# Kernel tuning notes

Hardware: AMD Instinct MI355X
Metric: run time of the kernel (lower is better)

The kernel has to match this reference:

```python
import jax, jax.numpy as jnp
import numpy as np

BS, V, S, K = 4, 2048, 7, 10
CLASS_NUM, VEC_NUM, CAT = 6, 8, 16
OUT_HEAD = CLASS_NUM + VEC_NUM * 3  # 30
DIM_FUSE = 128 + 128 + 256 + 256 + 512 + 512 + 16  # 1808


def _normalize(x, axis):
    return x / jnp.maximum(jnp.linalg.norm(x, axis=axis, keepdims=True), 1e-12)


def knn_index(verts, k):
    # verts: (b, v, 3) -> (b, v, k) excluding self
    inner = jnp.einsum('bnd,bmd->bnm', verts, verts)
    sq = jnp.sum(verts * verts, axis=2)
    dist = sq[:, :, None] + sq[:, None, :] - 2.0 * inner
    _, idx = jax.lax.top_k(-dist, k + 1)
    return idx[:, :, 1:]


def nearest_index(target, source):
    # target: (b, v1, 3), source: (b, v2, 3) -> (b, v1)
    inner = jnp.einsum('bnd,bmd->bnm', target, source)
    d = jnp.sum(source * source, 2)[:, None, :] + jnp.sum(target * target, 2)[:, :, None] - 2.0 * inner
    return jnp.argmin(d, axis=-1)


def gather_nb(t, idx):
    # t: (b, v, d), idx: (b, v1, k) -> (b, v1, k, d)
    return jax.vmap(lambda tt, ii: tt[ii])(t, idx)


def gather1(t, idx):
    # t: (b, v, d), idx: (b, v1) -> (b, v1, d)
    return jax.vmap(lambda tt, ii: tt[ii])(t, idx)


def bn_train(x, g, b, eps=1e-5):
    # x: (b, v, c); BatchNorm1d training-mode over (batch, vertices)
    m = jnp.mean(x, axis=(0, 1), keepdims=True)
    v = jnp.var(x, axis=(0, 1), keepdims=True)
    return (x - m) * jax.lax.rsqrt(v + eps) * g + b


def conv_surface(nb_idx, verts, directions, s, kernel_num):
    nd = _normalize(gather_nb(verts, nb_idx) - verts[:, :, None, :], -1)  # (b,v,n,3)
    sd = _normalize(directions, 0)  # (3, s*k)
    theta = jax.nn.relu(jnp.einsum('bvnd,dk->bvnk', nd, sd))
    b_, v_, n_, _ = theta.shape
    theta = theta.reshape(b_, v_, n_, s, kernel_num)
    return jnp.sum(jnp.max(theta, axis=2), axis=2)  # (b, v, kernel_num)


def conv_layer(nb_idx, verts, fm, w, b, directions, s, out_ch):
    nd = _normalize(gather_nb(verts, nb_idx) - verts[:, :, None, :], -1)
    sd = _normalize(directions, 0)  # (3, s*out_ch)
    theta = jax.nn.relu(jnp.einsum('bvnd,dk->bvnk', nd, sd))  # (b,v,n,s*o)
    fo = jnp.einsum('bvc,ck->bvk', fm, w) + b  # (b, v, (s+1)*o)
    center = fo[..., :out_ch]
    supp = gather_nb(fo[..., out_ch:], nb_idx)  # (b,v,n,s*o)
    act = (theta * supp).reshape(theta.shape[0], theta.shape[1], theta.shape[2], s, out_ch)
    act = jnp.sum(jnp.max(act, axis=2), axis=2)  # (b, v, o)
    return center + act


def pool_layer(verts, fm, pooling_rate, nb_num):
    idx = knn_index(verts, nb_num)
    pooled = jnp.max(gather_nb(fm, idx), axis=2)
    pool_num = verts.shape[1] // pooling_rate
    # deterministic subsample (torch uses randperm; fixed arange for reproducibility)
    return verts[:, :pool_num], pooled[:, :pool_num]


def setup_inputs() -> dict:
    key = jax.random.key(0)
    ks = jax.random.split(key, 16)
    def rn(i, shape, scale=0.05):
        return jax.random.normal(ks[i], shape, dtype=jnp.float32) * scale
    z = lambda *s: jnp.zeros(s, jnp.float32)
    o = lambda *s: jnp.ones(s, jnp.float32)
    return {
        'vertices': jax.random.normal(ks[0], (BS, V, 3), dtype=jnp.float32),
        'onehot': jax.nn.one_hot(jax.random.randint(ks[1], (BS,), 0, CAT), CAT, dtype=jnp.float32),
        'dir0': rn(2, (3, S * 128)),
        'w1': rn(3, (128, (S + 1) * 128)), 'b1': z((S + 1) * 128), 'dir1': rn(4, (3, S * 128)),
        'w2': rn(5, (128, (S + 1) * 256)), 'b2': z((S + 1) * 256), 'dir2': rn(6, (3, S * 256)),
        'w3': rn(7, (256, (S + 1) * 256)), 'b3': z((S + 1) * 256), 'dir3': rn(8, (3, S * 256)),
        'w4': rn(9, (256, (S + 1) * 512)), 'b4': z((S + 1) * 512), 'dir4': rn(10, (3, S * 512)),
        'g_bn1': o(128), 'be_bn1': z(128),
        'g_bn2': o(256), 'be_bn2': z(256),
        'g_bn3': o(256), 'be_bn3': z(256),
        'wc1': rn(11, (512, DIM_FUSE)), 'bc1': z(512),
        'wc2': rn(12, (512, 512)), 'bc2': z(512),
        'wc3': rn(13, (OUT_HEAD, 512)), 'bc3': z(OUT_HEAD),
    }


def reference(vertices, onehot, dir0, w1, b1, dir1, w2, b2, dir2, w3, b3, dir3,
              w4, b4, dir4, g_bn1, be_bn1, g_bn2, be_bn2, g_bn3, be_bn3,
              wc1, bc1, wc2, bc2, wc3, bc3):
    bs, v_num, _ = vertices.shape
    nb = knn_index(vertices, K)
    fm0 = jax.nn.relu(conv_surface(nb, vertices, dir0, S, 128))
    fm1 = jax.nn.relu(bn_train(conv_layer(nb, vertices, fm0, w1, b1, dir1, S, 128), g_bn1, be_bn1))
    vp1, fp1 = pool_layer(vertices, fm1, 4, 4)
    nb1 = knn_index(vp1, min(K, vp1.shape[1] // 8))
    fm2 = jax.nn.relu(bn_train(conv_layer(nb1, vp1, fp1, w2, b2, dir2, S, 256), g_bn2, be_bn2))
    fm3 = jax.nn.relu(bn_train(conv_layer(nb1, vp1, fm2, w3, b3, dir3, S, 256), g_bn3, be_bn3))
    vp2, fp2 = pool_layer(vp1, fm3, 4, 4)
    nb2 = knn_index(vp2, min(K, vp2.shape[1] // 8))
    fm4 = conv_layer(nb2, vp2, fp2, w4, b4, dir4, S, 512)
    f_global = jnp.max(fm4, axis=1)  # (b, 512)
    n1 = nearest_index(vertices, vp1)
    n2 = nearest_index(vertices, vp2)
    fm2u = gather1(fm2, n1)
    fm3u = gather1(fm3, n1)
    fm4u = gather1(fm4, n2)
    fg = jnp.broadcast_to(f_global[:, None, :], (bs, v_num, 512))
    oh = jnp.broadcast_to(onehot[:, None, :], (bs, v_num, CAT))
    feat = jnp.concatenate([fm0, fm1, fm2u, fm3u, fm4u, oh], axis=2)
    fuse = jnp.concatenate([fm0, fm1, fm2u, fm3u, fm4u, fg, oh], axis=2)
    h = jax.nn.relu(jnp.einsum('bvc,oc->bvo', fuse, wc1) + bc1)
    h = jax.nn.relu(jnp.einsum('bvc,oc->bvo', h, wc2) + bc2)
    pred = jnp.einsum('bvc,oc->bvo', h, wc3) + bc3
    seg = pred[..., :CLASS_NUM]
    vecs = pred[..., CLASS_NUM:CLASS_NUM + VEC_NUM * 3]
    return (seg, vecs, feat)
```

## Files before the change

### kernel.cpp

```cpp
#include <hip/hip_runtime.h>
#include <hip/hip_bf16.h>
#include <math.h>

#define BSZ 4
#define VN 2048
#define SS 7
#define KNB 10

typedef __attribute__((ext_vector_type(8))) short short8;
typedef __attribute__((ext_vector_type(4))) float f32x4;
typedef __attribute__((address_space(1))) const void gcvoid;
typedef __attribute__((address_space(3))) void lvoid;

__device__ inline ushort f2bf(float x) {
    __hip_bfloat16 h = __float2bfloat16(x);
    return *(ushort*)&h;
}

__device__ inline void gl2lds16(const ushort* g, ushort* l) {
    __builtin_amdgcn_global_load_lds((gcvoid*)g, (lvoid*)l, 16, 0, 0);
}

__device__ inline unsigned fenc(float f) {
    unsigned b = __float_as_uint(f);
    return (b & 0x80000000u) ? ~b : (b | 0x80000000u);
}
__device__ inline float fdec(unsigned e) {
    unsigned b = (e & 0x80000000u) ? (e & 0x7FFFFFFFu) : ~e;
    return __uint_as_float(b);
}

#define INS(dq, iq, dd, jj) { bool lt_ = (dd) < (dq); \
    float dmn_ = lt_ ? (dd) : (dq); float dmx_ = lt_ ? (dq) : (dd); \
    int imn_ = lt_ ? (jj) : (iq); int imx_ = lt_ ? (iq) : (jj); \
    (dq) = dmn_; (iq) = imn_; (dd) = dmx_; (jj) = imx_; }

#define PB0 8960L
#define PB1 24320L
#define PB2 958208L
#define PB3 1220352L

__global__ void prep_uber(const float* __restrict__ d0, const float* __restrict__ d1,
                          const float* __restrict__ d2, const float* __restrict__ d3,
                          const float* __restrict__ d4,
                          float* __restrict__ s0, float* __restrict__ s1,
                          float* __restrict__ s2, float* __restrict__ s3, float* __restrict__ s4,
                          const float* __restrict__ wc3, float* __restrict__ wc3t,
                          const float* __restrict__ wc1, ushort* __restrict__ wc1b,
                          const float* __restrict__ wc2, ushort* __restrict__ wc2b) {
    long i = blockIdx.x * 256L + threadIdx.x;
    if (i < PB0) {
        const float* src; float* dst; int C, c;
        if (i < 896)        { src = d0; dst = s0; C = 896;  c = (int)i; }
        else if (i < 1792)  { src = d1; dst = s1; C = 896;  c = (int)i - 896; }
        else if (i < 3584)  { src = d2; dst = s2; C = 1792; c = (int)i - 1792; }
        else if (i < 5376)  { src = d3; dst = s3; C = 1792; c = (int)i - 3584; }
        else                { src = d4; dst = s4; C = 3584; c = (int)i - 5376; }
        float a = src[c], b = src[C + c], e = src[2 * C + c];
        float den = fmaxf(sqrtf(a * a + b * b + e * e), 1e-12f);
        dst[c] = a / den; dst[C + c] = b / den; dst[2 * C + c] = e / den;
    } else if (i < PB1) {
        long j = i - PB0;
        int o = (int)(j / 512), k = (int)(j % 512);
        wc3t[(long)k * 30 + o] = wc3[j];
    } else if (i < PB2) {
        long j = i - PB1;
        int c = (int)(j % 1824);
        long r = j / 1824;
        wc1b[j] = f2bf(c < 1808 ? wc1[r * 1808 + c] : 0.f);
    } else if (i < PB3) {
        long j = i - PB2;
        wc2b[j] = f2bf(wc2[j]);
    }
}

__global__ __launch_bounds__(256) void wt_trans_all(const float* __restrict__ w1, const float* __restrict__ w2,
                                                    const float* __restrict__ w3, const float* __restrict__ w4,
                                                    ushort* __restrict__ o1, ushort* __restrict__ o2,
                                                    ushort* __restrict__ o3, ushort* __restrict__ o4) {
    __shared__ float tile[32][33];
    int gb = blockIdx.x;
    const float* w; ushort* o; int K, N, t;
    if (gb < 128)      { w = w1; o = o1; K = 128; N = 1024; t = gb; }
    else if (gb < 384) { w = w2; o = o2; K = 128; N = 2048; t = gb - 128; }
    else if (gb < 896) { w = w3; o = o3; K = 256; N = 2048; t = gb - 384; }
    else               { w = w4; o = o4; K = 256; N = 4096; t = gb - 896; }
    int tn = t % (N / 32), tk = t / (N / 32);
    int n0 = tn * 32, k0 = tk * 32;
    int tx = threadIdx.x % 32, ty = threadIdx.x / 32;
#pragma unroll
    for (int r = 0; r < 32; r += 8)
        tile[ty + r][tx] = w[(long)(k0 + ty + r) * N + n0 + tx];
    __syncthreads();
#pragma unroll
    for (int r = 0; r < 32; r += 8)
        o[(long)(n0 + ty + r) * K + k0 + tx] = f2bf(tile[tx][ty + r]);
}

#define KOFF0 0L
#define KOFF1 5242880L
#define KOFF2 5570560L
#define KTOT  5591040L

__device__ void knn_part_dev(const float* __restrict__ verts, int T, int nch,
                             int tile, int b, int ch,
                             float* __restrict__ pd, ushort* __restrict__ pi,
                             float4* __restrict__ s4) {
    const float* vb = verts + (long)b * VN * 3;
    int j0 = ch * 128;
    for (int j = threadIdx.x; j < 128; j += 256) {
        float x = vb[(j0 + j) * 3 + 0];
        float y = vb[(j0 + j) * 3 + 1];
        float z = vb[(j0 + j) * 3 + 2];
        s4[j] = make_float4(x, y, z, x * x + y * y + z * z);
    }
    __syncthreads();
    int i = tile * 256 + (int)threadIdx.x;
    if (i >= T) return;
    float px = vb[i * 3], py = vb[i * 3 + 1], pz = vb[i * 3 + 2];
    float d0[10], d1[10], d2[10], d3[10];
    int id0[10], id1[10], id2[10], id3[10];
#pragma unroll
    for (int q = 0; q < 10; q++) {
        d0[q] = 1e30f; d1[q] = 1e30f; d2[q] = 1e30f; d3[q] = 1e30f;
        id0[q] = 0; id1[q] = 0; id2[q] = 0; id3[q] = 0;
    }
    for (int j = 0; j < 32; j++) {
        float4 sA = s4[j];
        float4 sB = s4[32 + j];
        float4 sC = s4[64 + j];
        float4 sD = s4[96 + j];
        float dA = fmaf(-2.f, px * sA.x + py * sA.y + pz * sA.z, sA.w);
        float dB = fmaf(-2.f, px * sB.x + py * sB.y + pz * sB.z, sB.w);
        float dC = fmaf(-2.f, px * sC.x + py * sC.y + pz * sC.z, sC.w);
        float dD = fmaf(-2.f, px * sD.x + py * sD.y + pz * sD.z, sD.w);
        int jA = j0 + j, jB = j0 + 32 + j, jC = j0 + 64 + j, jD = j0 + 96 + j;
        dA = (jA == i) ? 1e30f : dA;
        dB = (jB == i) ? 1e30f : dB;
        dC = (jC == i) ? 1e30f : dC;
        dD = (jD == i) ? 1e30f : dD;
#pragma unroll
        for (int q = 0; q < 10; q++) { INS(d0[q], id0[q], dA, jA); }
#pragma unroll
        for (int q = 0; q < 10; q++) { INS(d1[q], id1[q], dB, jB); }
#pragma unroll
        for (int q = 0; q < 10; q++) { INS(d2[q], id2[q], dC, jC); }
#pragma unroll
        for (int q = 0; q < 10; q++) { INS(d3[q], id3[q], dD, jD); }
    }
    long base = ((long)(b * T + i) * nch + ch) * 40;
#pragma unroll
    for (int q = 0; q < 10; q++) { pd[base + q] = d0[q];      pi[base + q] = (ushort)id0[q]; }
#pragma unroll
    for (int q = 0; q < 10; q++) { pd[base + 10 + q] = d1[q]; pi[base + 10 + q] = (ushort)id1[q]; }
#pragma unroll
    for (int q = 0; q < 10; q++) { pd[base + 20 + q] = d2[q]; pi[base + 20 + q] = (ushort)id2[q]; }
#pragma unroll
    for (int q = 0; q < 10; q++) { pd[base + 30 + q] = d3[q]; pi[base + 30 + q] = (ushort)id3[q]; }
}

__device__ void nearest_dev(const float* __restrict__ verts, int SN, int* __restrict__ out,
                            int gl, float4* __restrict__ s4) {
    int t = gl * 256 + (int)threadIdx.x;
    int b = t / VN;
    const float* vb = verts + (long)b * VN * 3;
    for (int j = threadIdx.x; j < SN; j += 256) {
        float x = vb[j * 3], y = vb[j * 3 + 1], z = vb[j * 3 + 2];
        s4[j] = make_float4(x, y, z, x * x + y * y + z * z);
    }
    __syncthreads();
    int i = t % VN;
    float px = vb[i * 3], py = vb[i * 3 + 1], pz = vb[i * 3 + 2];
    int h = SN / 2;
    float b0 = 1e30f, b1 = 1e30f; int i0 = 0, i1 = 0;
    for (int j = 0; j < h; j++) {
        float4 sA = s4[j];
        float4 sB = s4[h + j];
        float dA = fmaf(-2.f, px * sA.x + py * sA.y + pz * sA.z, sA.w);
        float dB = fmaf(-2.f, px * sB.x + py * sB.y + pz * sB.z, sB.w);
        bool lA = dA < b0; b0 = lA ? dA : b0; i0 = lA ? j : i0;
        bool lB = dB < b1; b1 = lB ? dB : b1; i1 = lB ? (h + j) : i1;
    }
    out[t] = (b1 < b0) ? i1 : i0;
}

__global__ __launch_bounds__(256) void knn_part_uber(const float* __restrict__ verts,
                                                     float* __restrict__ pd, ushort* __restrict__ pi,
                                                     int* __restrict__ n1, int* __restrict__ n2) {
    __shared__ float4 smem[512];
    int gb = blockIdx.x;
    if (gb < 512) {
        int tile = gb & 7, bc = gb >> 3;
        knn_part_dev(verts, 2048, 16, tile, bc >> 4, bc & 15, pd + KOFF0, pi + KOFF0, smem);
    } else if (gb < 544) {
        int local = gb - 512;
        int tile = local & 1, bc = local >> 1;
        knn_part_dev(verts, 512, 4, tile, bc >> 2, bc & 3, pd + KOFF1, pi + KOFF1, smem);
    } else if (gb < 548) {
        int local = gb - 544;
        knn_part_dev(verts, 128, 1, 0, local, 0, pd + KOFF2, pi + KOFF2, smem);
    } else if (gb < 580) {
        nearest_dev(verts, 512, n1, gb - 548, smem);
    } else {
        nearest_dev(verts, 128, n2, gb - 580, smem);
    }
}

template <int NL>
__device__ void knn_merge_dev(const float* __restrict__ pd, const ushort* __restrict__ pi,
                              int blk, int Tb,
                              int* __restrict__ out, int* __restrict__ outp, int Tp,
                              float* sdl, int* sil) {
    int tgt = threadIdx.x >> 3;
    int sub = threadIdx.x & 7;
    long t = (long)blk * 32 + tgt;
    constexpr int GRP = (NL + 7) / 8;
    float d[10]; int id[10];
#pragma unroll
    for (int q = 0; q < 10; q++) { d[q] = 1e30f; id[q] = 0; }
    int c0 = sub * GRP;
    int c1 = (c0 + GRP < NL) ? c0 + GRP : NL;
    for (int c = c0; c < c1; c++) {
        long base = (t * NL + c) * 10;
        for (int q = 0; q < 10; q++) {
            float dd = pd[base + q];
            if (dd >= d[9]) break;
            int jj = (int)pi[base + q];
#pragma unroll
            for (int p = 0; p < 10; p++) { INS(d[p], id[p], dd, jj); }
        }
    }
    float* md = sdl + (tgt * 8 + sub) * 10;
    int* mi = sil + (tgt * 8 + sub) * 10;
#pragma unroll
    for (int q = 0; q < 10; q++) { md[q] = d[q]; mi[q] = id[q]; }
    __syncthreads();
    if (sub == 0) {
        for (int s = 1; s < 8; s++) {
            const float* od = sdl + (tgt * 8 + s) * 10;
            const int* oi = sil + (tgt * 8 + s) * 10;
            for (int q = 0; q < 10; q++) {
                float dd = od[q];
                if (dd >= d[9]) break;
                int jj = oi[q];
#pragma unroll
                for (int p = 0; p < 10; p++) { INS(d[p], id[p], dd, jj); }
            }
        }
#pragma unroll
        for (int q = 0; q < 10; q++) out[t * 10 + q] = id[q];
        if (outp) {
            int b = (int)(t / Tb), i = (int)(t % Tb);
            if (i < Tp) {
#pragma unroll
                for (int q = 0; q < 4; q++)
                    outp[((long)b * Tp + i) * 4 + q] = id[q];
            }
        }
    }
}

__global__ __launch_bounds__(256) void knn_merge_uber(const float* __restrict__ pd, const ushort* __restrict__ pi,
                                                      int* __restrict__ nb, int* __restrict__ nb1,
                                                      int* __restrict__ nb2, int* __restrict__ nbp1,
                                                      int* __restrict__ nbp2) {
    __shared__ float sdl[32 * 8 * 10];
    __shared__ int   sil[32 * 8 * 10];
    int gb = blockIdx.x;
    if (gb < 256)      knn_merge_dev<64>(pd + KOFF0, pi + KOFF0, gb, 2048, nb, nbp1, 512, sdl, sil);
    else if (gb < 320) knn_merge_dev<16>(pd + KOFF1, pi + KOFF1, gb - 256, 512, nb1, nbp2, 128, sdl, sil);
    else               knn_merge_dev<4>(pd + KOFF2, pi + KOFF2, gb - 320, 128, nb2, nullptr, 1, sdl, sil);
}

__global__ void conv_surface_kernel(const float* __restrict__ verts, const int* __restrict__ nb,
                                    const float* __restrict__ sd, float* __restrict__ fm0,
                                    ushort* __restrict__ fm0b) {
    int bv = blockIdx.x;
    int b = bv / VN, v = bv % VN;
    __shared__ float snd[KNB][3];
    int tid = threadIdx.x;
    if (tid < KNB) {
        int nj = nb[(long)bv * KNB + tid];
        const float* vb = verts + (long)b * VN * 3;
        float dx = vb[nj * 3] - vb[v * 3];
        float dy = vb[nj * 3 + 1] - vb[v * 3 + 1];
        float dz = vb[nj * 3 + 2] - vb[v * 3 + 2];
        float den = fmaxf(sqrtf(dx * dx + dy * dy + dz * dz), 1e-12f);
        snd[tid][0] = dx / den; snd[tid][1] = dy / den; snd[tid][2] = dz / den;
    }
    __syncthreads();
    int c = tid;
    float acc = 0.f;
    for (int s = 0; s < SS; s++) {
        int col = s * 128 + c;
        float s0 = sd[col], s1 = sd[896 + col], s2 = sd[2 * 896 + col];
        float m = 0.f;
#pragma unroll
        for (int n = 0; n < KNB; n++) {
            float dot = snd[n][0] * s0 + snd[n][1] * s1 + snd[n][2] * s2;
            m = fmaxf(m, dot);
        }
        acc += m;
    }
    fm0[(long)bv * 128 + c] = acc;
    fm0b[(long)bv * 128 + c] = f2bf(acc);
}

__global__ void conv_act_kernel(const float* __restrict__ verts, const int* __restrict__ nb,
                                const float* __restrict__ sd, const float* __restrict__ fo,
                                float* __restrict__ out, unsigned* __restrict__ fgmax,
                                int Vl, int outC) {
    int bv = blockIdx.x;
    int b = bv / Vl, v = bv % Vl;
    __shared__ float snd[KNB][3];
    __shared__ int srow[KNB];
    int tid = threadIdx.x;
    if (tid < KNB) {
        int nj = nb[(long)bv * KNB + tid];
        srow[tid] = b * Vl + nj;
        const float* vb = verts + (long)b * VN * 3;
        float dx = vb[nj * 3] - vb[v * 3];
        float dy = vb[nj * 3 + 1] - vb[v * 3 + 1];
        float dz = vb[nj * 3 + 2] - vb[v * 3 + 2];
        float den = fmaxf(sqrtf(dx * dx + dy * dy + dz * dz), 1e-12f);
        snd[tid][0] = dx / den; snd[tid][1] = dy / den; snd[tid][2] = dz / den;
    }
    __syncthreads();
    int c = tid;
    int SC = SS * outC;
    int foN = SC + outC;
    float acc = fo[(long)bv * foN + c];
    for (int s = 0; s < SS; s++) {
        int col = s * outC + c;
        float s0 = sd[col], s1 = sd[SC + col], s2 = sd[2 * SC + col];
        float m = -1e30f;
#pragma unroll
        for (int n = 0; n < KNB; n++) {
            float dot = snd[n][0] * s0 + snd[n][1] * s1 + snd[n][2] * s2;
            float th = fmaxf(dot, 0.f);
            float sup = fo[(long)srow[n] * foN + outC + col];
            m = fmaxf(m, th * sup);
        }
        acc += m;
    }
    out[(long)bv * outC + c] = acc;
    if (fgmax) atomicMax(&fgmax[b * outC + c], fenc(acc));
}

__global__ __launch_bounds__(256) void bn_stat_kernel(const float* __restrict__ x,
                                                      float* __restrict__ stat, int R, int C) {
    int rp = 256 / C;
    int c = threadIdx.x % C;
    int rs = threadIdx.x / C;
    float s = 0.f, s2 = 0.f;
    for (long r = (long)blockIdx.x * rp + rs; r < R; r += (long)gridDim.x * rp) {
        float v = x[r * C + c];
        s += v; s2 += v * v;
    }
    atomicAdd(&stat[c], s);
    atomicAdd(&stat[C + c], s2);
}

__global__ void bn_apply_relu_kernel(const float* __restrict__ x, const float* __restrict__ stat,
                                     const float* __restrict__ g, const float* __restrict__ be,
                                     float* __restrict__ out, ushort* __restrict__ outb, int R, int C) {
    long i = blockIdx.x * 256L + threadIdx.x;
    if (i >= (long)R * C) return;
    int c = (int)(i % C);
    float mu = stat[c] / R;
    float var = stat[C + c] / R - mu * mu;
    var = fmaxf(var, 0.f);
    float y = (x[i] - mu) * rsqrtf(var + 1e-5f) * g[c] + be[c];
    y = fmaxf(y, 0.f);
    out[i] = y;
    if (outb) outb[i] = f2bf(y);
}

__global__ void pool_b_kernel(const float* __restrict__ fm, const int* __restrict__ idx,
                              ushort* __restrict__ out, int Vin, int T, int C) {
    long i = blockIdx.x * 256L + threadIdx.x;
    if (i >= (long)BSZ * T * C) return;
    int c = (int)(i % C);
    long bt = i / C;
    int b = (int)(bt / T), t = (int)(bt % T);
    const int* id = idx + ((long)b * T + t) * 4;
    float m = -1e30f;
#pragma unroll
    for (int n = 0; n < 4; n++)
        m = fmaxf(m, fm[((long)b * Vin + id[n]) * C + c]);
    out[i] = f2bf(m);
}

__global__ __launch_bounds__(256) void gemm_mfma_bt_kernel(
    const ushort* __restrict__ A, const ushort* __restrict__ Bt,
    const float* __restrict__ bias, float* __restrict__ Cf, ushort* __restrict__ Cb,
    int M, int N, int K, int relu)
{
    __shared__ ushort As[128 * 32];
    __shared__ ushort Bs[128 * 32];
    int t = threadIdx.x;
    int w = t >> 6, l = t & 63;
    int quad = l >> 4, lm = l & 15;
    int wm = w >> 1, wn = w & 1;
    long m0 = blockIdx.y * 128L;
    long n0 = blockIdx.x * 128L;
    int lr = t >> 2;
    int lk = (t & 3) * 8;
    f32x4 acc[4][4];
#pragma unroll
    for (int i = 0; i < 4; i++)
#pragma unroll
        for (int j = 0; j < 4; j++) acc[i][j] = (f32x4){0.f, 0.f, 0.f, 0.f};

    for (int k0 = 0; k0 < K; k0 += 32) {
        __syncthreads();
        gl2lds16(A + (m0 + lr) * K + k0 + lk, &As[lr * 32 + lk]);
        gl2lds16(A + (m0 + 64 + lr) * K + k0 + lk, &As[(64 + lr) * 32 + lk]);
        gl2lds16(Bt + (n0 + lr) * K + k0 + lk, &Bs[lr * 32 + lk]);
        gl2lds16(Bt + (n0 + 64 + lr) * K + k0 + lk, &Bs[(64 + lr) * 32 + lk]);
        __syncthreads();
        short8 af[4], bfr[4];
#pragma unroll
        for (int i = 0; i < 4; i++)
            af[i] = *(const short8*)&As[(wm * 64 + i * 16 + lm) * 32 + quad * 8];
#pragma unroll
        for (int j = 0; j < 4; j++)
            bfr[j] = *(const short8*)&Bs[(wn * 64 + j * 16 + lm) * 32 + quad * 8];
#pragma unroll
        for (int i = 0; i < 4; i++)
#pragma unroll
            for (int j = 0; j < 4; j++)
                acc[i][j] = __builtin_amdgcn_mfma_f32_16x16x32_bf16(af[i], bfr[j], acc[i][j], 0, 0, 0);
    }
#pragma unroll
    for (int i = 0; i < 4; i++) {
#pragma unroll
        for (int j = 0; j < 4; j++) {
            int n = (int)n0 + wn * 64 + j * 16 + lm;
            float bv = bias[n];
#pragma unroll
            for (int r = 0; r < 4; r++) {
                int m = (int)m0 + wm * 64 + i * 16 + quad * 4 + r;
                float v = acc[i][j][r] + bv;
                if (relu) v = fmaxf(v, 0.f);
                if (Cf) Cf[(long)m * N + n] = v;
                if (Cb) Cb[(long)m * N + n] = f2bf(v);
            }
        }
    }
}

__global__ __launch_bounds__(256) void gemm_mfma_bt64_kernel(
    const ushort* __restrict__ A, const ushort* __restrict__ Bt,
    const float* __restrict__ bias, float* __restrict__ Cf, ushort* __restrict__ Cb,
    int M, int N, int K, int relu)
{
    __shared__ ushort As[64 * 32];
    __shared__ ushort Bs[128 * 32];
    int t = threadIdx.x;
    int w = t >> 6, l = t & 63;
    int quad = l >> 4, lm = l & 15;
    int wm = w >> 1, wn = w & 1;
    long m0 = blockIdx.y * 64L;
    long n0 = blockIdx.x * 128L;
    int lr = t >> 2;
    int lk = (t & 3) * 8;
    f32x4 acc[2][4];
#pragma unroll
    for (int i = 0; i < 2; i++)
#pragma unroll
        for (int j = 0; j < 4; j++) acc[i][j] = (f32x4){0.f, 0.f, 0.f, 0.f};

    for (int k0 = 0; k0 < K; k0 += 32) {
        __syncthreads();
        gl2lds16(A + (m0 + lr) * K + k0 + lk, &As[lr * 32 + lk]);
        gl2lds16(Bt + (n0 + lr) * K + k0 + lk, &Bs[lr * 32 + lk]);
        gl2lds16(Bt + (n0 + 64 + lr) * K + k0 + lk, &Bs[(64 + lr) * 32 + lk]);
        __syncthreads();
        short8 af[2], bfr[4];
#pragma unroll
        for (int i = 0; i < 2; i++)
            af[i] = *(const short8*)&As[(wm * 32 + i * 16 + lm) * 32 + quad * 8];
#pragma unroll
        for (int j = 0; j < 4; j++)
            bfr[j] = *(const short8*)&Bs[(wn * 64 + j * 16 + lm) * 32 + quad * 8];
#pragma unroll
        for (int i = 0; i < 2; i++)
#pragma unroll
            for (int j = 0; j < 4; j++)
                acc[i][j] = __builtin_amdgcn_mfma_f32_16x16x32_bf16(af[i], bfr[j], acc[i][j], 0, 0, 0);
    }
#pragma unroll
    for (int i = 0; i < 2; i++) {
#pragma unroll
        for (int j = 0; j < 4; j++) {
            int n = (int)n0 + wn * 64 + j * 16 + lm;
            float bv = bias[n];
#pragma unroll
            for (int r = 0; r < 4; r++) {
                int m = (int)m0 + wm * 32 + i * 16 + quad * 4 + r;
                float v = acc[i][j][r] + bv;
                if (relu) v = fmaxf(v, 0.f);
                if (Cf) Cf[(long)m * N + n] = v;
                if (Cb) Cb[(long)m * N + n] = f2bf(v);
            }
        }
    }
}

__global__ __launch_bounds__(256) void wc3_kernel(const float* __restrict__ h2,
                                                  const float* __restrict__ wc3t,
                                                  const float* __restrict__ bc3,
                                                  float* __restrict__ out) {
    int r8 = threadIdx.x >> 5;
    int c = threadIdx.x & 31;
    long row = blockIdx.x * 8L + r8;
    const float* hr = h2 + row * 512;
    float acc = 0.f;
    if (c < 30) {
        for (int k = 0; k < 512; k++)
            acc += hr[k] * wc3t[k * 30 + c];
        acc += bc3[c];
        if (c < 6) out[row * 6 + c] = acc;
        else       out[49152 + row * 24 + (c - 6)] = acc;
    }
}

__global__ __launch_bounds__(256) void fuse_bf_kernel(
    const float* __restrict__ fm0, const float* __restrict__ fm1,
    const float* __restrict__ fm2, const float* __restrict__ fm3,
    const float* __restrict__ fm4, const unsigned* __restrict__ fg_enc,
    const float* __restrict__ onehot,
    const int* __restrict__ n1, const int* __restrict__ n2,
    ushort* __restrict__ fuse_b, float* __restrict__ feat) {
    long row = blockIdx.x;
    int b = (int)(row >> 11);
    int i1 = n1[row], i2 = n2[row];
    const float* p0 = fm0 + row * 128;
    const float* p1 = fm1 + row * 128;
    const float* p2 = fm2 + ((long)b * 512 + i1) * 256;
    const float* p3 = fm3 + ((long)b * 512 + i1) * 256;
    const float* p4 = fm4 + ((long)b * 128 + i2) * 512;
    const unsigned* pg = fg_enc + b * 512;
    const float* po = onehot + b * 16;
    ushort* fb = fuse_b + row * 1824;
    float* ft = feat + row * 1296;
#pragma unroll
    for (int k = 0; k < 8; k++) {
        int c = threadIdx.x + k * 256;
        if (c >= 1824) break;
        float val = 0.f;
        if (c < 128)       val = p0[c];
        else if (c < 256)  val = p1[c - 128];
        else if (c < 512)  val = p2[c - 256];
        else if (c < 768)  val = p3[c - 512];
        else if (c < 1280) val = p4[c - 768];
        else if (c < 1792) val = fdec(pg[c - 1280]);
        else if (c < 1808) val = po[c - 1792];
        fb[c] = f2bf(val);
        if (c < 1280)                   ft[c] = val;
        else if (c >= 1792 && c < 1808) ft[c - 512] = val;
    }
}


extern "C" void kernel_launch(void* const* d_in, const int* in_sizes, int n_in,
                              void* d_out, int out_size, void* d_ws, size_t ws_size,
                              hipStream_t stream) {
    const float* verts  = (const float*)d_in[0];
    const float* onehot = (const float*)d_in[1];
    const float* dir0 = (const float*)d_in[2];
    const float* w1 = (const float*)d_in[3];
    const float* b1 = (const float*)d_in[4];
    const float* dir1 = (const float*)d_in[5];
    const float* w2 = (const float*)d_in[6];
    const float* b2 = (const float*)d_in[7];
    const float* dir2 = (const float*)d_in[8];
    const float* w3 = (const float*)d_in[9];
    const float* b3 = (const float*)d_in[10];
    const float* dir3 = (const float*)d_in[11];
    const float* w4 = (const float*)d_in[12];
    const float* b4 = (const float*)d_in[13];
    const float* dir4 = (const float*)d_in[14];
    const float* g_bn1 = (const float*)d_in[15];
    const float* be_bn1 = (const float*)d_in[16];
    const float* g_bn2 = (const float*)d_in[17];
    const float* be_bn2 = (const float*)d_in[18];
    const float* g_bn3 = (const float*)d_in[19];
    const float* be_bn3 = (const float*)d_in[20];
    const float* wc1 = (const float*)d_in[21];
    const float* bc1 = (const float*)d_in[22];
    const float* wc2 = (const float*)d_in[23];
    const float* bc2 = (const float*)d_in[24];
    const float* wc3 = (const float*)d_in[25];
    const float* bc3 = (const float*)d_in[26];
    float* outf = (float*)d_out;

    float* wsf = (float*)d_ws;
    size_t off = 0;
    auto alloc = [&](size_t n) { float* p = wsf + off; off += (n + 15) & ~(size_t)15; return p; };

    float* sd0 = alloc(3 * 896);
    float* sd1 = alloc(3 * 896);
    float* sd2 = alloc(3 * 1792);
    float* sd3 = alloc(3 * 1792);
    float* sd4 = alloc(3 * 3584);
    float* wc3t = alloc(512L * 30);
    float* fm0 = alloc(8192L * 128);
    float* fm1 = alloc(8192L * 128);
    float* c1  = alloc(8192L * 128);
    float* fm2 = alloc(2048L * 256);
    float* c2  = alloc(2048L * 256);
    float* fm3 = alloc(2048L * 256);
    float* c3  = alloc(2048L * 256);
    float* fm4 = alloc(512L * 512);
    float* statbase = alloc(3328);
    float* stat1 = statbase;
    float* stat2 = statbase + 256;
    float* stat3 = statbase + 768;
    unsigned* fg_enc = (unsigned*)(statbase + 1280);
    float* fbuf = alloc(8192L * 1024);
    float* h2 = alloc(8192L * 512);
    float* pd  = alloc(KTOT);
    ushort* pi = (ushort*)alloc(KTOT / 2);
    int* nb   = (int*)alloc(8192L * KNB);
    int* nb1  = (int*)alloc(2048L * KNB);
    int* nb2  = (int*)alloc(512L * KNB);
    int* nbp1 = (int*)alloc(2048L * 4);
    int* nbp2 = (int*)alloc(512L * 4);
    int* n1   = (int*)alloc(8192);
    int* n2   = (int*)alloc(8192);
    ushort* fuse_b = (ushort*)alloc(8192L * 1824 / 2);
    ushort* h1b    = (ushort*)alloc(8192L * 512 / 2);
    ushort* wc1b   = (ushort*)alloc(512L * 1824 / 2);
    ushort* wc2b   = (ushort*)alloc(512L * 512 / 2);
    ushort* w1tb   = (ushort*)alloc(1024L * 128 / 2);
    ushort* w2tb   = (ushort*)alloc(2048L * 128 / 2);
    ushort* w3tb   = (ushort*)alloc(2048L * 256 / 2);
    ushort* w4tb   = (ushort*)alloc(4096L * 256 / 2);
    ushort* fm0b   = (ushort*)alloc(8192L * 128 / 2);
    ushort* fp1b   = (ushort*)alloc(2048L * 128 / 2);
    ushort* fm2b   = (ushort*)alloc(2048L * 256 / 2);
    ushort* fp2b   = (ushort*)alloc(512L * 256 / 2);

    auto nblk = [](long n, int b) { return (unsigned)((n + b - 1) / b); };

    hipMemsetAsync(statbase, 0, 3328 * sizeof(float), stream);
    prep_uber<<<nblk(PB3, 256), 256, 0, stream>>>(dir0, dir1, dir2, dir3, dir4,
                                                  sd0, sd1, sd2, sd3, sd4,
                                                  wc3, wc3t, wc1, wc1b, wc2, wc2b);
    wt_trans_all<<<1920, 256, 0, stream>>>(w1, w2, w3, w4, w1tb, w2tb, w3tb, w4tb);

    knn_part_uber<<<612, 256, 0, stream>>>(verts, pd, pi, n1, n2);
    knn_merge_uber<<<336, 256, 0, stream>>>(pd, pi, nb, nb1, nb2, nbp1, nbp2);

    conv_surface_kernel<<<BSZ * 2048, 128, 0, stream>>>(verts, nb, sd0, fm0, fm0b);

    gemm_mfma_bt_kernel<<<dim3(8, 64), 256, 0, stream>>>(fm0b, w1tb, b1, fbuf, nullptr, 8192, 1024, 128, 0);
    conv_act_kernel<<<BSZ * 2048, 128, 0, stream>>>(verts, nb, sd1, fbuf, c1, nullptr, 2048, 128);
    bn_stat_kernel<<<256, 256, 0, stream>>>(c1, stat1, 8192, 128);
    bn_apply_relu_kernel<<<nblk(8192L * 128, 256), 256, 0, stream>>>(c1, stat1, g_bn1, be_bn1, fm1, nullptr, 8192, 128);

    pool_b_kernel<<<nblk(BSZ * 512L * 128, 256), 256, 0, stream>>>(fm1, nbp1, fp1b, 2048, 512, 128);

    gemm_mfma_bt64_kernel<<<dim3(16, 32), 256, 0, stream>>>(fp1b, w2tb, b2, fbuf, nullptr, 2048, 2048, 128, 0);
    conv_act_kernel<<<BSZ * 512, 256, 0, stream>>>(verts, nb1, sd2, fbuf, c2, nullptr, 512, 256);
    bn_stat_kernel<<<256, 256, 0, stream>>>(c2, stat2, 2048, 256);
    bn_apply_relu_kernel<<<nblk(2048L * 256, 256), 256, 0, stream>>>(c2, stat2, g_bn2, be_bn2, fm2, fm2b, 2048, 256);

    gemm_mfma_bt64_kernel<<<dim3(16, 32), 256, 0, stream>>>(fm2b, w3tb, b3, fbuf, nullptr, 2048, 2048, 256, 0);
    conv_act_kernel<<<BSZ * 512, 256, 0, stream>>>(verts, nb1, sd3, fbuf, c3, nullptr, 512, 256);
    bn_stat_kernel<<<256, 256, 0, stream>>>(c3, stat3, 2048, 256);
    bn_apply_relu_kernel<<<nblk(2048L * 256, 256), 256, 0, stream>>>(c3, stat3, g_bn3, be_bn3, fm3, nullptr, 2048, 256);

    pool_b_kernel<<<nblk(BSZ * 128L * 256, 256), 256, 0, stream>>>(fm3, nbp2, fp2b, 512, 128, 256);

    gemm_mfma_bt64_kernel<<<dim3(32, 8), 256, 0, stream>>>(fp2b, w4tb, b4, fbuf, nullptr, 512, 4096, 256, 0);
    conv_act_kernel<<<BSZ * 128, 512, 0, stream>>>(verts, nb2, sd4, fbuf, fm4, fg_enc, 128, 512);

    fuse_bf_kernel<<<8192, 256, 0, stream>>>(fm0, fm1, fm2, fm3, fm4, fg_enc, onehot,
                                             n1, n2, fuse_b, outf + 245760);

    gemm_mfma_bt64_kernel<<<dim3(4, 128), 256, 0, stream>>>(fuse_b, wc1b, bc1, nullptr, h1b, 8192, 512, 1824, 1);
    gemm_mfma_bt64_kernel<<<dim3(4, 128), 256, 0, stream>>>(h1b, wc2b, bc2, h2, nullptr, 8192, 512, 512, 1);
    wc3_kernel<<<1024, 256, 0, stream>>>(h2, wc3t, bc3, outf);
}
```

Before: 505.8 us.

## Replace serial KNN partial-list merge with warp-shuffle tournament selection

The KNN merge step now gives each partial top-10 list its own thread instead of having 8 threads scan several lists and one thread merge them through shared memory. Distance and index are packed into a 64-bit key, and the 10 smallest keys are pulled out with xor-shuffle min reductions, advancing each thread's sorted list. This drops the serial insertion sorts, the LDS staging and the block barrier, and launches many more blocks. In exchange every lane reads all its candidates, and each output needs 10 reduction rounds of 64-bit shuffles.

```diff
diff --git a/kernel.cpp b/kernel.cpp
--- a/kernel.cpp
+++ b/kernel.cpp
@@ -206,56 +206,49 @@
     }
 }
 
-template <int NL>
-__device__ void knn_merge_dev(const float* __restrict__ pd, const ushort* __restrict__ pi,
-                              int blk, int Tb,
-                              int* __restrict__ out, int* __restrict__ outp, int Tp,
-                              float* sdl, int* sil) {
-    int tgt = threadIdx.x >> 3;
-    int sub = threadIdx.x & 7;
-    long t = (long)blk * 32 + tgt;
-    constexpr int GRP = (NL + 7) / 8;
-    float d[10]; int id[10];
-#pragma unroll
-    for (int q = 0; q < 10; q++) { d[q] = 1e30f; id[q] = 0; }
-    int c0 = sub * GRP;
-    int c1 = (c0 + GRP < NL) ? c0 + GRP : NL;
-    for (int c = c0; c < c1; c++) {
-        long base = (t * NL + c) * 10;
-        for (int q = 0; q < 10; q++) {
-            float dd = pd[base + q];
-            if (dd >= d[9]) break;
-            int jj = (int)pi[base + q];
-#pragma unroll
-            for (int p = 0; p < 10; p++) { INS(d[p], id[p], dd, jj); }
+template <int G>
+__device__ void knn_sel_dev(const float* __restrict__ pd, const ushort* __restrict__ pi,
+                            int blk, int Tb, int* __restrict__ out,
+                            int* __restrict__ outp, int Tp) {
+    typedef unsigned long long u64;
+    constexpr int TPB = 256 / G;
+    int tid = threadIdx.x;
+    long t = (long)blk * TPB + (tid / G);
+    int c = tid % G;
+    long base = (t * G + c) * 10;
+    const float2* pf = (const float2*)(pd + base);
+    const uint*   pu = (const uint*)(pi + base);
+    float2 f0 = pf[0], f1 = pf[1], f2 = pf[2], f3 = pf[3], f4 = pf[4];
+    uint   u0 = pu[0], u1 = pu[1], u2 = pu[2], u3 = pu[3], u4 = pu[4];
+    u64 k0 = ((u64)fenc(f0.x) << 32) | (u0 & 0xFFFFu);
+    u64 k1 = ((u64)fenc(f0.y) << 32) | (u0 >> 16);
+    u64 k2 = ((u64)fenc(f1.x) << 32) | (u1 & 0xFFFFu);
+    u64 k3 = ((u64)fenc(f1.y) << 32) | (u1 >> 16);
+    u64 k4 = ((u64)fenc(f2.x) << 32) | (u2 & 0xFFFFu);
+    u64 k5 = ((u64)fenc(f2.y) << 32) | (u2 >> 16);
+    u64 k6 = ((u64)fenc(f3.x) << 32) | (u3 & 0xFFFFu);
+    u64 k7 = ((u64)fenc(f3.y) << 32) | (u3 >> 16);
+    u64 k8 = ((u64)fenc(f4.x) << 32) | (u4 & 0xFFFFu);
+    u64 k9 = ((u64)fenc(f4.y) << 32) | (u4 >> 16);
+    int bb = (int)(t / Tb), ii = (int)(t % Tb);
+    bool wp = (outp != nullptr) && (ii < Tp);
+#pragma unroll
+    for (int q = 0; q < 10; q++) {
+        u64 m = k0;
+#pragma unroll
+        for (int s = 1; s < G; s <<= 1) {
+            u64 o = (u64)__shfl_xor((long long)m, s);
+            m = (o < m) ? o : m;
         }
-    }
-    float* md = sdl + (tgt * 8 + sub) * 10;
-    int* mi = sil + (tgt * 8 + sub) * 10;
-#pragma unroll
-    for (int q = 0; q < 10; q++) { md[q] = d[q]; mi[q] = id[q]; }
-    __syncthreads();
-    if (sub == 0) {
-        for (int s = 1; s < 8; s++) {
-            const float* od = sdl + (tgt * 8 + s) * 10;
-            const int* oi = sil + (tgt * 8 + s) * 10;
-            for (int q = 0; q < 10; q++) {
-                float dd = od[q];
-                if (dd >= d[9]) break;
-                int jj = oi[q];
-#pragma unroll
-                for (int p = 0; p < 10; p++) { INS(d[p], id[p], dd, jj); }
-            }
+        if (c == 0) {
+            int idx = (int)(unsigned)(m & 0xFFFFFFFFull);
+            out[t * 10 + q] = idx;
+            if (wp && q < 4) outp[((long)bb * Tp + ii) * 4 + q] = idx;
         }
-#pragma unroll
-        for (int q = 0; q < 10; q++) out[t * 10 + q] = id[q];
-        if (outp) {
-            int b = (int)(t / Tb), i = (int)(t % Tb);
-            if (i < Tp) {
-#pragma unroll
-                for (int q = 0; q < 4; q++)
-                    outp[((long)b * Tp + i) * 4 + q] = id[q];
-            }
+        if (k0 == m) {
+            k0 = k1; k1 = k2; k2 = k3; k3 = k4; k4 = k5;
+            k5 = k6; k6 = k7; k7 = k8; k8 = k9;
+            k9 = 0xFFFFFFFFFFFFFFFFull;
         }
     }
 }
@@ -264,12 +257,10 @@
                                                       int* __restrict__ nb, int* __restrict__ nb1,
                                                       int* __restrict__ nb2, int* __restrict__ nbp1,
                                                       int* __restrict__ nbp2) {
-    __shared__ float sdl[32 * 8 * 10];
-    __shared__ int   sil[32 * 8 * 10];
     int gb = blockIdx.x;
-    if (gb < 256)      knn_merge_dev<64>(pd + KOFF0, pi + KOFF0, gb, 2048, nb, nbp1, 512, sdl, sil);
-    else if (gb < 320) knn_merge_dev<16>(pd + KOFF1, pi + KOFF1, gb - 256, 512, nb1, nbp2, 128, sdl, sil);
-    else               knn_merge_dev<4>(pd + KOFF2, pi + KOFF2, gb - 320, 128, nb2, nullptr, 1, sdl, sil);
+    if (gb < 2048)      knn_sel_dev<64>(pd + KOFF0, pi + KOFF0, gb, 2048, nb, nbp1, 512);
+    else if (gb < 2176) knn_sel_dev<16>(pd + KOFF1, pi + KOFF1, gb - 2048, 512, nb1, nbp2, 128);
+    else                knn_sel_dev<4>(pd + KOFF2, pi + KOFF2, gb - 2176, 128, nb2, nullptr, 1);
 }
 
 __global__ void conv_surface_kernel(const float* __restrict__ verts, const int* __restrict__ nb,
@@ -652,7 +643,7 @@
     wt_trans_all<<<1920, 256, 0, stream>>>(w1, w2, w3, w4, w1tb, w2tb, w3tb, w4tb);
 
     knn_part_uber<<<612, 256, 0, stream>>>(verts, pd, pi, n1, n2);
-    knn_merge_uber<<<336, 256, 0, stream>>>(pd, pi, nb, nb1, nb2, nbp1, nbp2);
+    knn_merge_uber<<<2184, 256, 0, stream>>>(pd, pi, nb, nb1, nb2, nbp1, nbp2);
 
     conv_surface_kernel<<<BSZ * 2048, 128, 0, stream>>>(verts, nb, sd0, fm0, fm0b);
 
```

Result: faster. 469.6 us (-7.2%).
